# Performance work log

Hardware: AMD Instinct MI355X
Metric: run time of the kernel (lower is better)

## Reference

```python
import jax, jax.numpy as jnp
import numpy as np

N_NODES = 100000
N_EDGES = 1600000
IN_DIM = 128
HID = 64


def _init_linear(key, fan_in, fan_out):
    kw, kb = jax.random.split(key)
    bound = 1.0 / np.sqrt(fan_in)
    W = jax.random.uniform(kw, (fan_in, fan_out), jnp.float32, -bound, bound)
    b = jax.random.uniform(kb, (fan_out,), jnp.float32, -bound, bound)
    return W, b


def setup_inputs() -> dict:
    key = jax.random.key(0)
    ks = jax.random.split(key, 6)
    x = jax.random.normal(ks[0], (N_NODES, IN_DIM), jnp.float32)
    edge_index = jax.random.randint(ks[1], (2, N_EDGES), 0, N_NODES, jnp.int64)
    W_pre, b_pre = _init_linear(ks[2], IN_DIM, HID)
    W1, b1 = _init_linear(ks[3], HID, HID)
    W2, b2 = _init_linear(ks[4], HID, HID)
    W3, b3 = _init_linear(ks[5], HID, HID)
    return {"x": x, "edge_index": edge_index, "W_pre": W_pre, "b_pre": b_pre,
            "W1": W1, "b1": b1, "W2": W2, "b2": b2, "W3": W3, "b3": b3}


def _gcn_layer(h, src, dst, dinv, W, b):
    # PyG GCNConv: h' = D^{-1/2} (A + I) D^{-1/2} (h W) + b, deg from A+I
    n = h.shape[0]
    hw = h @ W                                  # [N, out]
    norm = dinv[src] * dinv[dst]                # [E]
    msg = hw[src] * norm[:, None]               # gather + scale  [E, out]
    agg = jax.ops.segment_sum(msg, dst, num_segments=n)  # scatter-add
    agg = agg + hw * (dinv * dinv)[:, None]     # self-loop term (norm = dinv_i^2)
    return agg + b


def reference(x, edge_index, W_pre, b_pre, W1, b1, W2, b2, W3, b3):
    src, dst = edge_index[0], edge_index[1]
    n = x.shape[0]
    # degree of A + I (self loops added, as in GCNConv default)
    deg = jax.ops.segment_sum(jnp.ones(src.shape[0], x.dtype), dst, num_segments=n) + 1.0
    dinv = jax.lax.rsqrt(deg)

    h = x @ W_pre + b_pre                       # feature_pre linear
    h = jax.nn.relu(_gcn_layer(h, src, dst, dinv, W1, b1))  # dropout is identity in eval
    h = jax.nn.relu(_gcn_layer(h, src, dst, dinv, W2, b2))
    h = _gcn_layer(h, src, dst, dinv, W3, b3)
    # F.normalize(p=2, dim=-1) with eps=1e-12
    nrm = jnp.linalg.norm(h, axis=-1, keepdims=True)
    return h / jnp.maximum(nrm, 1e-12)
```

## Files before the change

kernel.cpp:

```cpp
#include <hip/hip_runtime.h>

#define N_NODES 100000
#define N_EDGES 1600000
#define IN_DIM 128
#define HID 64
#define NB 782
#define NBLK_GEMM 782
#define NGROUP 25000

typedef __attribute__((ext_vector_type(8))) _Float16 h8v;
typedef __attribute__((ext_vector_type(4))) float f4v;

struct Args {
  const float* x; const int* ei;
  const float* Wp; const float* bp;
  const float* W1; const float* b1;
  const float* W2; const float* b2;
  const float* W3; const float* b3;
  float* out;
  _Float16* bufA16; _Float16* hw16;
  int* pairs; int* csr; int* offs; float* dinv;
  int* bsz; int* bboff; int* bcur;
  _Float16* WpH; _Float16* WpL; _Float16* W1H; _Float16* W1L;
  _Float16* W2H; _Float16* W2L; _Float16* W3H; _Float16* W3L;
};

__device__ __forceinline__ void d_split(const float* __restrict__ W,
                                        _Float16* __restrict__ hi,
                                        _Float16* __restrict__ lo, int K, int i) {
  int k = i >> 6, n = i & 63;
  float v = W[i];
  _Float16 h = (_Float16)v;
  float r = v - (float)h;
  hi[n * K + k] = h;
  lo[n * K + k] = (_Float16)r;
}

__global__ __launch_bounds__(256) void f_prep(Args a) {
  int blk = blockIdx.x, t = threadIdx.x;
  if (blk < 32) d_split(a.Wp, a.WpH, a.WpL, IN_DIM, blk * 256 + t);
  else if (blk < 48) d_split(a.W1, a.W1H, a.W1L, HID, (blk - 32) * 256 + t);
  else if (blk < 64) d_split(a.W2, a.W2H, a.W2L, HID, (blk - 48) * 256 + t);
  else d_split(a.W3, a.W3H, a.W3L, HID, (blk - 64) * 256 + t);
}

__global__ __launch_bounds__(256) void f_bhist(Args a) {
  __shared__ int cnt[NB];
  int t = threadIdx.x;
  for (int i = t; i < NB; i += 256) cnt[i] = 0;
  __syncthreads();
  int e0 = blockIdx.x * 8192, e1 = min(e0 + 8192, N_EDGES);
  for (int e = e0 + t; e < e1; e += 256)
    atomicAdd(&cnt[a.ei[N_EDGES + e] >> 7], 1);
  __syncthreads();
  for (int i = t; i < NB; i += 256)
    if (cnt[i]) atomicAdd(&a.bsz[i], cnt[i]);
}

__global__ __launch_bounds__(256) void f_bscan(Args a) {
  __shared__ int sm[256];
  int t = threadIdx.x;
  int c[4];
  int idx0 = t * 4;
#pragma unroll
  for (int j = 0; j < 4; ++j) c[j] = (idx0 + j < NB) ? a.bsz[idx0 + j] : 0;
  int tsum = c[0] + c[1] + c[2] + c[3];
  int val = tsum;
  sm[t] = val;
  __syncthreads();
  for (int off = 1; off < 256; off <<= 1) {
    int u = (t >= off) ? sm[t - off] : 0;
    __syncthreads();
    val += u;
    sm[t] = val;
    __syncthreads();
  }
  int excl = val - tsum;
#pragma unroll
  for (int j = 0; j < 4; ++j) {
    int idx = idx0 + j;
    if (idx < NB) { a.bboff[idx] = excl; a.bcur[idx] = excl; }
    excl += c[j];
  }
  if (t == 255) a.bboff[NB] = val;
}

__global__ __launch_bounds__(256) void f_partition(Args a) {
  __shared__ int cnt[NB];
  __shared__ int base[NB];
  int t = threadIdx.x;
  for (int i = t; i < NB; i += 256) cnt[i] = 0;
  __syncthreads();
  int e0 = blockIdx.x * 8192, e1 = min(e0 + 8192, N_EDGES);
  for (int e = e0 + t; e < e1; e += 256)
    atomicAdd(&cnt[a.ei[N_EDGES + e] >> 7], 1);
  __syncthreads();
  for (int i = t; i < NB; i += 256) {
    int c = cnt[i];
    base[i] = c ? atomicAdd(&a.bcur[i], c) : 0;
    cnt[i] = 0;
  }
  __syncthreads();
  for (int e = e0 + t; e < e1; e += 256) {
    int s = a.ei[e];
    int d = a.ei[N_EDGES + e];
    int b = d >> 7;
    int r = atomicAdd(&cnt[b], 1);
    a.pairs[base[b] + r] = ((d & 127) << 17) | s;
  }
}

__global__ __launch_bounds__(256) void f_csrdeg(Args a) {
  __shared__ int ldeg[128];
  __shared__ int sc[128];
  __shared__ int lcur[128];
  int t = threadIdx.x;
  int b = blockIdx.x;
  int node0 = b << 7;
  int nloc = min(128, N_NODES - node0);
  int beg = a.bboff[b], end = a.bboff[b + 1];
  if (t < 128) ldeg[t] = 0;
  __syncthreads();
  for (int i = beg + t; i < end; i += 256)
    atomicAdd(&ldeg[(a.pairs[i] >> 17) & 127], 1);
  __syncthreads();
  int dv = (t < 128) ? ldeg[t] : 0;
  if (t < 128) sc[t] = dv;
  __syncthreads();
  for (int off = 1; off < 128; off <<= 1) {
    int u = (t >= off && t < 128) ? sc[t - off] : 0;
    __syncthreads();
    if (t < 128) sc[t] += u;
    __syncthreads();
  }
  if (t < nloc) {
    int o = beg + sc[t] - dv;
    a.offs[node0 + t] = o;
    lcur[t] = o;
    a.dinv[node0 + t] = rsqrtf((float)dv + 1.0f);
  }
  if (b == NB - 1 && t == 0) a.offs[N_NODES] = N_EDGES;
  __syncthreads();
  for (int i = beg + t; i < end; i += 256) {
    int p = a.pairs[i];
    int pos = atomicAdd(&lcur[(p >> 17) & 127], 1);
    a.csr[pos] = p & 131071;
  }
}

__global__ __launch_bounds__(256) void f_gemm_pre(Args a) {
  __shared__ _Float16 sW[2 * 64 * IN_DIM];
  int t = threadIdx.x;
  int wave = t >> 6, lane = t & 63, fi = lane & 15, quad = lane >> 4;
  int r0 = blockIdx.x * 128 + wave * 32;

  f4v xb0[8], xb1[8];
  {
    int row = r0 + fi; if (row >= N_NODES) row = N_NODES - 1;
    const float* xp = a.x + (size_t)row * IN_DIM + quad * 8;
#pragma unroll
    for (int j = 0; j < 4; ++j) {
      xb0[2 * j]     = *(const f4v*)(xp + j * 32);
      xb0[2 * j + 1] = *(const f4v*)(xp + j * 32 + 4);
    }
  }
#pragma unroll
  for (int i = 0; i < 8; ++i) {
    int c = i * 256 + t;
    int h = c >> 10;
    int c2 = c & 1023;
    int n = c2 >> 4;
    const _Float16* src = (h ? a.WpL : a.WpH) + c2 * 8;
    f4v v = *(const f4v*)src;
    int off = (h << 14) | ((c2 * 16) ^ ((n & 7) << 4));
    *(f4v*)((char*)sW + off) = v;
  }
  __syncthreads();

  float bv[4];
#pragma unroll
  for (int ct = 0; ct < 4; ++ct) bv[ct] = a.bp[ct * 16 + fi];

#pragma unroll
  for (int f = 0; f < 2; ++f) {
    f4v* xcur = (f & 1) ? xb1 : xb0;
    f4v* xnxt = (f & 1) ? xb0 : xb1;
    if (f < 1) {
      int row = r0 + 16 + fi; if (row >= N_NODES) row = N_NODES - 1;
      const float* xp = a.x + (size_t)row * IN_DIM + quad * 8;
#pragma unroll
      for (int j = 0; j < 4; ++j) {
        xnxt[2 * j]     = *(const f4v*)(xp + j * 32);
        xnxt[2 * j + 1] = *(const f4v*)(xp + j * 32 + 4);
      }
    }
    f4v acc[4];
#pragma unroll
    for (int ct = 0; ct < 4; ++ct) acc[ct] = (f4v){0.f, 0.f, 0.f, 0.f};
#pragma unroll
    for (int k0i = 0; k0i < 4; ++k0i) {
      h8v ah, al;
#pragma unroll
      for (int j = 0; j < 4; ++j) {
        float v0 = xcur[2 * k0i][j], v1 = xcur[2 * k0i + 1][j];
        _Float16 h0 = (_Float16)v0, h1 = (_Float16)v1;
        ah[j] = h0;     al[j] = (_Float16)(v0 - (float)h0);
        ah[4 + j] = h1; al[4 + j] = (_Float16)(v1 - (float)h1);
      }
#pragma unroll
      for (int ct = 0; ct < 4; ++ct) {
        int n = ct * 16 + fi;
        int bo = ((n * IN_DIM + k0i * 32 + quad * 8) * 2) ^ ((n & 7) << 4);
        h8v bh = *(const h8v*)((const char*)sW + bo);
        h8v bl = *(const h8v*)((const char*)sW + 16384 + bo);
        acc[ct] = __builtin_amdgcn_mfma_f32_16x16x32_f16(ah, bh, acc[ct], 0, 0, 0);
        acc[ct] = __builtin_amdgcn_mfma_f32_16x16x32_f16(al, bh, acc[ct], 0, 0, 0);
        acc[ct] = __builtin_amdgcn_mfma_f32_16x16x32_f16(ah, bl, acc[ct], 0, 0, 0);
      }
    }
    int ro = r0 + f * 16;
#pragma unroll
    for (int ct = 0; ct < 4; ++ct) {
#pragma unroll
      for (int j = 0; j < 4; ++j) {
        int orow = ro + quad * 4 + j;
        if (orow < N_NODES)
          a.bufA16[(size_t)orow * HID + ct * 16 + fi] = (_Float16)(acc[ct][j] + bv[ct]);
      }
    }
  }
}

__global__ __launch_bounds__(256) void f_gemm64(Args a, const _Float16* __restrict__ Wh,
                                                const _Float16* __restrict__ Wl) {
  int t = threadIdx.x;
  int wave = t >> 6, lane = t & 63, fi = lane & 15, quad = lane >> 4;
  int r0 = blockIdx.x * 128 + wave * 32;

  h8v a0[2], a1[2];
  {
    int row = r0 + fi; if (row >= N_NODES) row = N_NODES - 1;
    const _Float16* xp = a.bufA16 + (size_t)row * HID + quad * 8;
    a0[0] = *(const h8v*)xp;
    a0[1] = *(const h8v*)(xp + 32);
  }
  h8v Bh[2][4], Bl[2][4];
#pragma unroll
  for (int k0i = 0; k0i < 2; ++k0i)
#pragma unroll
    for (int ct = 0; ct < 4; ++ct) {
      size_t o = (size_t)(ct * 16 + fi) * HID + k0i * 32 + quad * 8;
      Bh[k0i][ct] = *(const h8v*)(Wh + o);
      Bl[k0i][ct] = *(const h8v*)(Wl + o);
    }

#pragma unroll
  for (int f = 0; f < 2; ++f) {
    h8v* av = (f & 1) ? a1 : a0;
    h8v* nx = (f & 1) ? a0 : a1;
    if (f < 1) {
      int row = r0 + 16 + fi; if (row >= N_NODES) row = N_NODES - 1;
      const _Float16* xp = a.bufA16 + (size_t)row * HID + quad * 8;
      nx[0] = *(const h8v*)xp;
      nx[1] = *(const h8v*)(xp + 32);
    }
    f4v acc[4];
#pragma unroll
    for (int ct = 0; ct < 4; ++ct) acc[ct] = (f4v){0.f, 0.f, 0.f, 0.f};
#pragma unroll
    for (int k0i = 0; k0i < 2; ++k0i)
#pragma unroll
      for (int ct = 0; ct < 4; ++ct) {
        acc[ct] = __builtin_amdgcn_mfma_f32_16x16x32_f16(av[k0i], Bh[k0i][ct], acc[ct], 0, 0, 0);
        acc[ct] = __builtin_amdgcn_mfma_f32_16x16x32_f16(av[k0i], Bl[k0i][ct], acc[ct], 0, 0, 0);
      }
    int ro = r0 + f * 16;
#pragma unroll
    for (int ct = 0; ct < 4; ++ct)
#pragma unroll
      for (int j = 0; j < 4; ++j) {
        int orow = ro + quad * 4 + j;
        if (orow < N_NODES)
          a.hw16[(size_t)orow * HID + ct * 16 + fi] = (_Float16)acc[ct][j];
      }
  }
}

template <int MODE>
__device__ __forceinline__ void d_agg(int grp, const _Float16* __restrict__ hw,
                                      const int* __restrict__ offs,
                                      const int* __restrict__ csr,
                                      const float* __restrict__ dinv,
                                      const float* __restrict__ bias,
                                      _Float16* __restrict__ out16,
                                      float* __restrict__ out32) {
  int node = grp * 4 + (threadIdx.x >> 6);
  int lane = threadIdx.x & 63;
  float di = dinv[node];
  int beg = offs[node];
  int end = offs[node + 1];
  int deg = end - beg;
  float bv = bias[lane];

  _Float16 hself = hw[(size_t)node * HID + lane];
  float acc = (float)hself * (di * di);

  for (int c0 = 0; c0 < deg; c0 += 64) {
    int nc = min(64, deg - c0);
    int ei = beg + c0 + ((lane < nc) ? lane : (nc - 1));
    int sv = csr[ei];
    float wv = (lane < nc) ? dinv[sv] * di : 0.0f;

    int rn = (nc + 7) & ~7;
    for (int j = 0; j < rn; j += 8) {
      _Float16 v[8];
      float wj[8];
#pragma unroll
      for (int u = 0; u < 8; ++u) {
        int sj = __builtin_amdgcn_readlane(sv, j + u);
        wj[u] = __int_as_float(__builtin_amdgcn_readlane(__float_as_int(wv), j + u));
        const _Float16* p = hw + ((size_t)sj << 6);
        v[u] = p[lane];
      }
#pragma unroll
      for (int u = 0; u < 8; ++u) acc += (float)v[u] * wj[u];
    }
  }

  acc += bv;
  if (MODE == 0) {
    out16[(size_t)node * HID + lane] = (_Float16)fmaxf(acc, 0.f);
  } else {
    float ss = acc * acc;
#pragma unroll
    for (int w = 1; w < 64; w <<= 1) ss += __shfl_xor(ss, w);
    float sc = 1.0f / fmaxf(sqrtf(ss), 1e-12f);
    out32[(size_t)node * HID + lane] = acc * sc;
  }
}

__global__ __launch_bounds__(256) void f_agg_relu(Args a, const float* bias) {
  d_agg<0>(blockIdx.x, a.hw16, a.offs, a.csr, a.dinv, bias, a.bufA16, nullptr);
}

__global__ __launch_bounds__(256) void f_agg_norm(Args a) {
  d_agg<1>(blockIdx.x, a.hw16, a.offs, a.csr, a.dinv, a.b3, nullptr, a.out);
}

extern "C" void kernel_launch(void* const* d_in, const int* in_sizes, int n_in,
                              void* d_out, int out_size, void* d_ws, size_t ws_size,
                              hipStream_t stream) {
  char* ws = (char*)d_ws;
  Args a;
  a.x  = (const float*)d_in[0];
  a.ei = (const int*)d_in[1];
  a.Wp = (const float*)d_in[2];  a.bp = (const float*)d_in[3];
  a.W1 = (const float*)d_in[4];  a.b1 = (const float*)d_in[5];
  a.W2 = (const float*)d_in[6];  a.b2 = (const float*)d_in[7];
  a.W3 = (const float*)d_in[8];  a.b3 = (const float*)d_in[9];
  a.out  = (float*)d_out;
  a.bufA16 = (_Float16*)(ws + 0);
  a.hw16   = (_Float16*)(ws + 12800000);
  a.pairs  = (int*)(ws + 25600000);
  a.csr    = (int*)(ws + 32000000);
  a.offs   = (int*)(ws + 38400000);
  a.dinv   = (float*)(ws + 38800016);
  a.bsz    = (int*)(ws + 39200016);
  a.bboff  = (int*)(ws + 39203152);
  a.bcur   = (int*)(ws + 39206288);
  a.WpH = (_Float16*)(ws + 39210000);
  a.WpL = (_Float16*)(ws + 39226384);
  a.W1H = (_Float16*)(ws + 39242768);
  a.W1L = (_Float16*)(ws + 39250960);
  a.W2H = (_Float16*)(ws + 39259152);
  a.W2L = (_Float16*)(ws + 39267344);
  a.W3H = (_Float16*)(ws + 39275536);
  a.W3L = (_Float16*)(ws + 39283728);

  (void)hipMemsetAsync(a.bsz, 0, NB * sizeof(int), stream);
  f_prep<<<80, 256, 0, stream>>>(a);
  f_bhist<<<196, 256, 0, stream>>>(a);
  f_bscan<<<1, 256, 0, stream>>>(a);
  f_partition<<<196, 256, 0, stream>>>(a);
  f_csrdeg<<<NB, 256, 0, stream>>>(a);
  f_gemm_pre<<<NBLK_GEMM, 256, 0, stream>>>(a);
  f_gemm64<<<NBLK_GEMM, 256, 0, stream>>>(a, a.W1H, a.W1L);
  f_agg_relu<<<NGROUP, 256, 0, stream>>>(a, a.b1);
  f_gemm64<<<NBLK_GEMM, 256, 0, stream>>>(a, a.W2H, a.W2L);
  f_agg_relu<<<NGROUP, 256, 0, stream>>>(a, a.b2);
  f_gemm64<<<NBLK_GEMM, 256, 0, stream>>>(a, a.W3H, a.W3L);
  f_agg_norm<<<NGROUP, 256, 0, stream>>>(a);
}
```

Baseline: 358.8 us.

## Precompute per-edge byte offset and weight array for GCN aggregation

Adds a pass that stores, for each CSR edge, the pre-shifted byte offset of the source row together with dinv[src]. The three aggregation kernels then read this int2 array directly instead of doing readlane broadcasts and an extra dinv gather. The inner loop now does 16-wide unrolled gathers with mixed-precision FMA, and the dst dinv is applied once at the end. The cost is one extra kernel and 12.8 MB of metadata that must be read on every layer.

```diff
diff --git a/kernel.cpp b/kernel.cpp
--- a/kernel.cpp
+++ b/kernel.cpp
@@ -21,6 +21,7 @@
   _Float16* bufA16; _Float16* hw16;
   int* pairs; int* csr; int* offs; float* dinv;
   int* bsz; int* bboff; int* bcur;
+  int2* meta;
   _Float16* WpH; _Float16* WpL; _Float16* W1H; _Float16* W1L;
   _Float16* W2H; _Float16* W2L; _Float16* W3H; _Float16* W3L;
 };
@@ -144,8 +145,16 @@
   for (int i = beg + t; i < end; i += 256) {
     int p = a.pairs[i];
     int pos = atomicAdd(&lcur[(p >> 17) & 127], 1);
-    a.csr[pos] = p & 131071;
-  }
+    a.csr[pos] = (p & 131071) << 7;
+  }
+}
+
+__global__ __launch_bounds__(256) void f_wgt(Args a) {
+  int e = blockIdx.x * 256 + threadIdx.x;
+  if (e >= N_EDGES) return;
+  int off = a.csr[e];
+  float w = a.dinv[off >> 7];
+  a.meta[e] = make_int2(off, __float_as_int(w));
 }
 
 __global__ __launch_bounds__(256) void f_gemm_pre(Args a) {
@@ -289,45 +298,63 @@
 template <int MODE>
 __device__ __forceinline__ void d_agg(int grp, const _Float16* __restrict__ hw,
                                       const int* __restrict__ offs,
-                                      const int* __restrict__ csr,
+                                      const int2* __restrict__ meta,
                                       const float* __restrict__ dinv,
                                       const float* __restrict__ bias,
                                       _Float16* __restrict__ out16,
                                       float* __restrict__ out32) {
   int node = grp * 4 + (threadIdx.x >> 6);
   int lane = threadIdx.x & 63;
+  int beg = __builtin_amdgcn_readfirstlane(offs[node]);
+  int end = __builtin_amdgcn_readfirstlane(offs[node + 1]);
+  int deg = end - beg;
   float di = dinv[node];
-  int beg = offs[node];
-  int end = offs[node + 1];
-  int deg = end - beg;
-  float bv = bias[lane];
-
-  _Float16 hself = hw[(size_t)node * HID + lane];
-  float acc = (float)hself * (di * di);
-
-  for (int c0 = 0; c0 < deg; c0 += 64) {
-    int nc = min(64, deg - c0);
-    int ei = beg + c0 + ((lane < nc) ? lane : (nc - 1));
-    int sv = csr[ei];
-    float wv = (lane < nc) ? dinv[sv] * di : 0.0f;
-
-    int rn = (nc + 7) & ~7;
-    for (int j = 0; j < rn; j += 8) {
-      _Float16 v[8];
-      float wj[8];
-#pragma unroll
-      for (int u = 0; u < 8; ++u) {
-        int sj = __builtin_amdgcn_readlane(sv, j + u);
-        wj[u] = __int_as_float(__builtin_amdgcn_readlane(__float_as_int(wv), j + u));
-        const _Float16* p = hw + ((size_t)sj << 6);
-        v[u] = p[lane];
-      }
-#pragma unroll
-      for (int u = 0; u < 8; ++u) acc += (float)v[u] * wj[u];
-    }
-  }
-
-  acc += bv;
+
+  float acc = 0.f;
+  {
+    unsigned hs = *(const unsigned short*)((const char*)hw + ((size_t)node << 7) + lane * 2);
+    asm("v_fma_mix_f32 %0, %1, %2, %0 op_sel:[0,0,0] op_sel_hi:[1,0,0]"
+        : "+v"(acc) : "v"(hs), "v"(di));
+  }
+
+  const int2* mp = meta + beg;
+  int lb = lane * 2;
+  int nfull = deg >> 4;
+  for (int b = 0; b < nfull; ++b) {
+    int2 mb[16];
+#pragma unroll
+    for (int u = 0; u < 16; ++u) mb[u] = mp[u];
+    unsigned hv[16];
+#pragma unroll
+    for (int u = 0; u < 16; ++u)
+      hv[u] = *(const unsigned short*)((const char*)hw + (unsigned)mb[u].x + lb);
+#pragma unroll
+    for (int u = 0; u < 16; ++u) {
+      float w = __int_as_float(mb[u].y);
+      asm("v_fma_mix_f32 %0, %1, %2, %0 op_sel:[0,0,0] op_sel_hi:[1,0,0]"
+          : "+v"(acc) : "v"(hv[u]), "v"(w));
+    }
+    mp += 16;
+  }
+  int rem = deg & 15;
+  if (rem) {
+    int2 mb[16];
+#pragma unroll
+    for (int u = 0; u < 16; ++u) mb[u] = mp[(u < rem) ? u : 0];
+    unsigned hv[16];
+#pragma unroll
+    for (int u = 0; u < 16; ++u)
+      hv[u] = *(const unsigned short*)((const char*)hw + (unsigned)mb[u].x + lb);
+#pragma unroll
+    for (int u = 0; u < 16; ++u) {
+      float w = (u < rem) ? __int_as_float(mb[u].y) : 0.0f;
+      asm("v_fma_mix_f32 %0, %1, %2, %0 op_sel:[0,0,0] op_sel_hi:[1,0,0]"
+          : "+v"(acc) : "v"(hv[u]), "v"(w));
+    }
+  }
+
+  acc *= di;
+  acc += bias[lane];
   if (MODE == 0) {
     out16[(size_t)node * HID + lane] = (_Float16)fmaxf(acc, 0.f);
   } else {
@@ -340,11 +367,11 @@
 }
 
 __global__ __launch_bounds__(256) void f_agg_relu(Args a, const float* bias) {
-  d_agg<0>(blockIdx.x, a.hw16, a.offs, a.csr, a.dinv, bias, a.bufA16, nullptr);
+  d_agg<0>(blockIdx.x, a.hw16, a.offs, a.meta, a.dinv, bias, a.bufA16, nullptr);
 }
 
 __global__ __launch_bounds__(256) void f_agg_norm(Args a) {
-  d_agg<1>(blockIdx.x, a.hw16, a.offs, a.csr, a.dinv, a.b3, nullptr, a.out);
+  d_agg<1>(blockIdx.x, a.hw16, a.offs, a.meta, a.dinv, a.b3, nullptr, a.out);
 }
 
 extern "C" void kernel_launch(void* const* d_in, const int* in_sizes, int n_in,
@@ -376,6 +403,7 @@
   a.W2L = (_Float16*)(ws + 39267344);
   a.W3H = (_Float16*)(ws + 39275536);
   a.W3L = (_Float16*)(ws + 39283728);
+  a.meta = (int2*)(ws + 40000000);
 
   (void)hipMemsetAsync(a.bsz, 0, NB * sizeof(int), stream);
   f_prep<<<80, 256, 0, stream>>>(a);
@@ -383,6 +411,7 @@
   f_bscan<<<1, 256, 0, stream>>>(a);
   f_partition<<<196, 256, 0, stream>>>(a);
   f_csrdeg<<<NB, 256, 0, stream>>>(a);
+  f_wgt<<<6250, 256, 0, stream>>>(a);
   f_gemm_pre<<<NBLK_GEMM, 256, 0, stream>>>(a);
   f_gemm64<<<NBLK_GEMM, 256, 0, stream>>>(a, a.W1H, a.W1L);
   f_agg_relu<<<NGROUP, 256, 0, stream>>>(a, a.b1);
```

Measured after the change: 457.6 us. +27.5%, slower.
